# Kernel tuning notes

Hardware: AMD Instinct MI355X
Metric: run time of the kernel (lower is better)

The kernel has to match this reference:

```python
import jax, jax.numpy as jnp
from jax import lax
import numpy as np

B, T, F, H = 2048, 256, 64, 32


def setup_inputs() -> dict:
    key = jax.random.key(0)
    k = jax.random.split(key, 7)
    s_ih = 1.0 / np.sqrt(H)  # PyTorch GRU init scale uniform(-1/sqrt(H), 1/sqrt(H))
    return {
        "x": jax.random.normal(k[0], (B, T, F), dtype=jnp.float32),
        "W_ih": jax.random.uniform(k[1], (3 * H, F), minval=-s_ih, maxval=s_ih, dtype=jnp.float32),
        "W_hh": jax.random.uniform(k[2], (3 * H, H), minval=-s_ih, maxval=s_ih, dtype=jnp.float32),
        "b_ih": jax.random.uniform(k[3], (3 * H,), minval=-s_ih, maxval=s_ih, dtype=jnp.float32),
        "b_hh": jax.random.uniform(k[4], (3 * H,), minval=-s_ih, maxval=s_ih, dtype=jnp.float32),
        "W_head": jax.random.uniform(k[5], (1, H), minval=-s_ih, maxval=s_ih, dtype=jnp.float32),
        "b_head": jax.random.uniform(k[6], (1,), minval=-s_ih, maxval=s_ih, dtype=jnp.float32),
    }


def _gru_last_hidden(x, W_ih, W_hh, b_ih, b_hh):
    # Precompute input-to-gate projections for all timesteps: [B,T,3H] -> [T,B,3H]
    xg = jnp.einsum("btf,gf->btg", x, W_ih) + b_ih
    xg = jnp.moveaxis(xg, 1, 0)

    def step(h, xt):
        hg = h @ W_hh.T + b_hh  # [B,3H]
        xr, xz, xn = jnp.split(xt, 3, axis=-1)  # PyTorch gate order: r, z, n
        hr, hz, hn = jnp.split(hg, 3, axis=-1)
        r = jax.nn.sigmoid(xr + hr)
        z = jax.nn.sigmoid(xz + hz)
        n = jnp.tanh(xn + r * hn)
        h_new = (1.0 - z) * n + z * h
        return h_new, None

    h0 = jnp.zeros((x.shape[0], W_hh.shape[1]), dtype=x.dtype)
    hT, _ = lax.scan(step, h0, xg)
    return hT  # [B,H] == out[:, -1, :]


def reference(x, W_ih, W_hh, b_ih, b_hh, W_head, b_head):
    hT = _gru_last_hidden(x, W_ih, W_hh, b_ih, b_hh)
    y = hT @ W_head.T + b_head  # [B,1]
    return jax.nn.sigmoid(y)
```

## Files before the change

kernel.cpp:

```cpp
#include <hip/hip_runtime.h>
#include <cstdint>


#define TSEQ 256

typedef __attribute__((ext_vector_type(8))) short bf16x8;
typedef __attribute__((ext_vector_type(4))) float f32x4;
union BF8 { unsigned u[4]; bf16x8 v; };

__device__ __forceinline__ unsigned bfr(float f) {
    unsigned u = __float_as_uint(f);
    return u + 0x7fffu + ((u >> 16) & 1u);
}
__device__ __forceinline__ unsigned packhi(unsigned a, unsigned b) {
    return __builtin_amdgcn_perm(b, a, 0x07060302u);
}
__device__ __forceinline__ void cvt2(const float4& f0, const float4& f1,
                                     bf16x8& hi, bf16x8& lo) {
    float f[8] = {f0.x,f0.y,f0.z,f0.w, f1.x,f1.y,f1.z,f1.w};
    BF8 H, L;
    #pragma unroll
    for (int d = 0; d < 4; ++d) {
        float a = f[2*d], b = f[2*d+1];
        unsigned ua = __float_as_uint(a), ub = __float_as_uint(b);
        float ra = a - __uint_as_float(ua & 0xffff0000u);
        float rb = b - __uint_as_float(ub & 0xffff0000u);
        H.u[d] = packhi(ua, ub);
        L.u[d] = packhi(bfr(ra), bfr(rb));
    }
    hi = H.v; lo = L.v;
}
__device__ __forceinline__ float sel4(f32x4 v, int u) {
    float a = (u & 1) ? v[1] : v[0];
    float b = (u & 1) ? v[3] : v[2];
    return (u & 2) ? b : a;
}
__device__ __forceinline__ float sigx(float v) {
    return __builtin_amdgcn_rcpf(1.f + exp2f(-1.4426950408889634f * v));
}
__device__ __forceinline__ float tanhx(float v) {
    float e = exp2f(-2.8853900817779268f * fabsf(v));
    return copysignf((1.f - e) * __builtin_amdgcn_rcpf(1.f + e), v);
}

#define MFMA16(A, B, C) __builtin_amdgcn_mfma_f32_16x16x32_bf16((A), (B), (C), 0, 0, 0)

__global__ __launch_bounds__(128, 1)
void gru_fused(const float* __restrict__ x, const float* __restrict__ W_ih,
               const float* __restrict__ W_hh, const float* __restrict__ b_ih,
               const float* __restrict__ b_hh, const float* __restrict__ W_head,
               const float* __restrict__ b_head, float* __restrict__ out)
{
    __shared__ float xsh[2][1536];
    const int tid  = threadIdx.x;
    const int wid  = tid >> 6;
    const int lane = tid & 63;
    const int m = lane & 15, q = lane >> 4;
    const int bq = m & 3, u = m >> 2;
    const int b0 = blockIdx.x * 4;

    bf16x8 Aih[6][2];
    float4 ring[4];
    const float* xcol = x + ((size_t)(b0 + bq)*TSEQ + u)*64 + q*8;
    auto ldring = [&](int grp) {
        const float* p = xcol + grp*256;
        ring[0] = ((const float4*)p)[0];        ring[1] = ((const float4*)p)[1];
        ring[2] = ((const float4*)(p+32))[0];   ring[3] = ((const float4*)(p+32))[1];
    };
    auto projwrite = [&](int buf) {
        bf16x8 Xh0, Xl0, Xh1, Xl1;
        cvt2(ring[0], ring[1], Xh0, Xl0);
        cvt2(ring[2], ring[3], Xh1, Xl1);
        #pragma unroll
        for (int nt = 0; nt < 6; ++nt) {
            f32x4 a = MFMA16(Aih[nt][0], Xh0, ((f32x4){0.f,0.f,0.f,0.f}));
            a = MFMA16(Aih[nt][0], Xl0, a);
            a = MFMA16(Aih[nt][1], Xh1, a);
            a = MFMA16(Aih[nt][1], Xl1, a);
            *(f32x4*)&xsh[buf][lane*24 + nt*4] = a;
        }
    };

    bf16x8 Awh[6];
    f32x4 FRZ[4], BN0, BN1;
    float fn0 = 0.f, fn1 = 0.f;
    unsigned Hd[4] = {0u, 0u, 0u, 0u};
    float hOL = 0.f, hOH = 0.f;

    if (wid == 1) {
        #pragma unroll
        for (int nt = 0; nt < 6; ++nt)
            #pragma unroll
            for (int c = 0; c < 2; ++c) {
                const float* wp = W_ih + (nt*16 + m)*64 + c*32 + q*8;
                BF8 t;
                #pragma unroll
                for (int d = 0; d < 4; ++d) t.u[d] = packhi(bfr(wp[2*d]), bfr(wp[2*d+1]));
                Aih[nt][c] = t.v;
            }
        ldring(0);
        projwrite(0);
        ldring(1);
    } else {
        #pragma unroll
        for (int nt = 0; nt < 6; ++nt) {
            const float* wp = W_hh + (nt*16 + m)*32;
            BF8 t;
            #pragma unroll
            for (int d = 0; d < 4; ++d) {
                int dd = q*4 + d;
                t.u[d] = packhi(bfr(wp[dd]), bfr(wp[dd + 16]));
            }
            Awh[nt] = t.v;
        }
        #pragma unroll
        for (int nt = 0; nt < 4; ++nt) {
            f32x4 t;
            #pragma unroll
            for (int r = 0; r < 4; ++r) { int g = nt*16 + q*4 + r; t[r] = b_ih[g] + b_hh[g]; }
            FRZ[nt] = t;
        }
        #pragma unroll
        for (int r = 0; r < 4; ++r) { BN0[r] = b_hh[64+q*4+r]; BN1[r] = b_hh[80+q*4+r]; }
        fn0 = b_ih[64 + q*4 + u]; fn1 = b_ih[80 + q*4 + u];
    }
    __syncthreads();

    const int s0 = (q << 4) + bq;
    for (int g = 0; g < 64; ++g) {
        if (wid == 1) {
            if (g < 63) {
                projwrite((g + 1) & 1);
                ldring(g + 2 < 64 ? g + 2 : 63);
            }
        } else {
            const int cbuf = g & 1;
            float xp[4][6];
            #pragma unroll
            for (int s = 0; s < 4; ++s) {
                const float* rp = &xsh[cbuf][(s0 + 4*s)*24 + u];
                #pragma unroll
                for (int nt = 0; nt < 6; ++nt) xp[s][nt] = rp[nt*4];
            }
            #pragma unroll
            for (int s = 0; s < 4; ++s) {
                BF8 bh; bh.u[0]=Hd[0]; bh.u[1]=Hd[1]; bh.u[2]=Hd[2]; bh.u[3]=Hd[3];
                f32x4 a0 = MFMA16(Awh[0], bh.v, FRZ[0]);
                f32x4 a1 = MFMA16(Awh[1], bh.v, FRZ[1]);
                f32x4 a2 = MFMA16(Awh[2], bh.v, FRZ[2]);
                f32x4 a3 = MFMA16(Awh[3], bh.v, FRZ[3]);
                f32x4 a4 = MFMA16(Awh[4], bh.v, BN0);
                f32x4 a5 = MFMA16(Awh[5], bh.v, BN1);

                float r0 = sigx(xp[s][0] + sel4(a0, u));
                float r1 = sigx(xp[s][1] + sel4(a1, u));
                float z0 = sigx(xp[s][2] + sel4(a2, u));
                float z1 = sigx(xp[s][3] + sel4(a3, u));
                float t0 = tanhx(xp[s][4] + fn0 + r0 * sel4(a4, u));
                float t1 = tanhx(xp[s][5] + fn1 + r1 * sel4(a5, u));
                float hNL = t0 + z0 * (hOL - t0);
                float hNH = t1 + z1 * (hOH - t1);
                hOL = hNL; hOH = hNH;

                unsigned pk = packhi(bfr(hNL), bfr(hNH));
                #pragma unroll
                for (int w = 0; w < 4; ++w)
                    Hd[w] = (unsigned)__shfl((int)pk, s0 + (w << 2), 64);
            }
        }
        __syncthreads();
    }

    if (wid == 0) {
        float v = hOL * W_head[q*4 + u] + hOH * W_head[16 + q*4 + u];
        v += __shfl_xor(v, 4, 64);
        v += __shfl_xor(v, 8, 64);
        v += __shfl_xor(v, 16, 64);
        v += __shfl_xor(v, 32, 64);
        if (lane < 4) out[b0 + lane] = sigx(v + b_head[0]);
    }
}

extern "C" void kernel_launch(void* const* d_in, const int* in_sizes, int n_in,
                              void* d_out, int out_size, void* d_ws, size_t ws_size,
                              hipStream_t stream)
{
    const float* x      = (const float*)d_in[0];
    const float* W_ih   = (const float*)d_in[1];
    const float* W_hh   = (const float*)d_in[2];
    const float* b_ih   = (const float*)d_in[3];
    const float* b_hh   = (const float*)d_in[4];
    const float* W_head = (const float*)d_in[5];
    const float* b_head = (const float*)d_in[6];
    float* out = (float*)d_out;

    gru_fused<<<512, 128, 0, stream>>>(x, W_ih, W_hh, b_ih, b_hh,
                                       W_head, b_head, out);
}
```

Baseline: 255.0 us.

## Drop per-step cross-lane shuffles by computing all four gate rows per lane

The projected-input buffer in LDS now uses the MFMA C-fragment layout, so the recurrent wave can read whole f32x4 vectors instead of scalar gathers. Each lane now evaluates the gate activations for all four accumulator rows of its column. That lets it build the next bf16 hidden-state B operand directly and removes the sel4 selection and the four __shfl exchanges per timestep. Barriers are replaced with one that waits only on lgkmcnt. The cost is four times more sigmoid/tanh work per lane, computed redundantly across lanes.

```diff
diff --git a/kernel.cpp b/kernel.cpp
--- a/kernel.cpp
+++ b/kernel.cpp
@@ -30,11 +30,6 @@
     }
     hi = H.v; lo = L.v;
 }
-__device__ __forceinline__ float sel4(f32x4 v, int u) {
-    float a = (u & 1) ? v[1] : v[0];
-    float b = (u & 1) ? v[3] : v[2];
-    return (u & 2) ? b : a;
-}
 __device__ __forceinline__ float sigx(float v) {
     return __builtin_amdgcn_rcpf(1.f + exp2f(-1.4426950408889634f * v));
 }
@@ -44,6 +39,12 @@
 }
 
 #define MFMA16(A, B, C) __builtin_amdgcn_mfma_f32_16x16x32_bf16((A), (B), (C), 0, 0, 0)
+
+__device__ __forceinline__ void barrier_nodrain() {
+    asm volatile("s_waitcnt lgkmcnt(0)" ::: "memory");
+    __builtin_amdgcn_s_barrier();
+    asm volatile("" ::: "memory");
+}
 
 __global__ __launch_bounds__(128, 1)
 void gru_fused(const float* __restrict__ x, const float* __restrict__ W_ih,
@@ -77,15 +78,15 @@
             a = MFMA16(Aih[nt][0], Xl0, a);
             a = MFMA16(Aih[nt][1], Xh1, a);
             a = MFMA16(Aih[nt][1], Xl1, a);
-            *(f32x4*)&xsh[buf][lane*24 + nt*4] = a;
+            *(f32x4*)&xsh[buf][nt*256 + lane*4] = a;
         }
     };
 
     bf16x8 Awh[6];
-    f32x4 FRZ[4], BN0, BN1;
-    float fn0 = 0.f, fn1 = 0.f;
+    f32x4 FRZ[4], BN0, BN1, FN0, FN1;
     unsigned Hd[4] = {0u, 0u, 0u, 0u};
-    float hOL = 0.f, hOH = 0.f;
+    float hL[4] = {0.f,0.f,0.f,0.f};
+    float hH[4] = {0.f,0.f,0.f,0.f};
 
     if (wid == 1) {
         #pragma unroll
@@ -121,10 +122,12 @@
             FRZ[nt] = t;
         }
         #pragma unroll
-        for (int r = 0; r < 4; ++r) { BN0[r] = b_hh[64+q*4+r]; BN1[r] = b_hh[80+q*4+r]; }
-        fn0 = b_ih[64 + q*4 + u]; fn1 = b_ih[80 + q*4 + u];
-    }
-    __syncthreads();
+        for (int r = 0; r < 4; ++r) {
+            BN0[r] = b_hh[64+q*4+r]; BN1[r] = b_hh[80+q*4+r];
+            FN0[r] = b_ih[64+q*4+r]; FN1[r] = b_ih[80+q*4+r];
+        }
+    }
+    barrier_nodrain();
 
     const int s0 = (q << 4) + bq;
     for (int g = 0; g < 64; ++g) {
@@ -135,13 +138,13 @@
             }
         } else {
             const int cbuf = g & 1;
-            float xp[4][6];
-            #pragma unroll
-            for (int s = 0; s < 4; ++s) {
-                const float* rp = &xsh[cbuf][(s0 + 4*s)*24 + u];
+            f32x4 xpv[4][6];
+            #pragma unroll
+            for (int s = 0; s < 4; ++s)
                 #pragma unroll
-                for (int nt = 0; nt < 6; ++nt) xp[s][nt] = rp[nt*4];
-            }
+                for (int nt = 0; nt < 6; ++nt)
+                    xpv[s][nt] = *(const f32x4*)&xsh[cbuf][nt*256 + (s0 + 4*s)*4];
+
             #pragma unroll
             for (int s = 0; s < 4; ++s) {
                 BF8 bh; bh.u[0]=Hd[0]; bh.u[1]=Hd[1]; bh.u[2]=Hd[2]; bh.u[3]=Hd[3];
@@ -152,29 +155,29 @@
                 f32x4 a4 = MFMA16(Awh[4], bh.v, BN0);
                 f32x4 a5 = MFMA16(Awh[5], bh.v, BN1);
 
-                float r0 = sigx(xp[s][0] + sel4(a0, u));
-                float r1 = sigx(xp[s][1] + sel4(a1, u));
-                float z0 = sigx(xp[s][2] + sel4(a2, u));
-                float z1 = sigx(xp[s][3] + sel4(a3, u));
-                float t0 = tanhx(xp[s][4] + fn0 + r0 * sel4(a4, u));
-                float t1 = tanhx(xp[s][5] + fn1 + r1 * sel4(a5, u));
-                float hNL = t0 + z0 * (hOL - t0);
-                float hNH = t1 + z1 * (hOH - t1);
-                hOL = hNL; hOH = hNH;
-
-                unsigned pk = packhi(bfr(hNL), bfr(hNH));
                 #pragma unroll
-                for (int w = 0; w < 4; ++w)
-                    Hd[w] = (unsigned)__shfl((int)pk, s0 + (w << 2), 64);
-            }
-        }
-        __syncthreads();
+                for (int r = 0; r < 4; ++r) {
+                    float rL = sigx(xpv[s][0][r] + a0[r]);
+                    float rH = sigx(xpv[s][1][r] + a1[r]);
+                    float zL = sigx(xpv[s][2][r] + a2[r]);
+                    float zH = sigx(xpv[s][3][r] + a3[r]);
+                    float tL = tanhx(xpv[s][4][r] + FN0[r] + rL * a4[r]);
+                    float tH = tanhx(xpv[s][5][r] + FN1[r] + rH * a5[r]);
+                    float nL = tL + zL * (hL[r] - tL);
+                    float nH = tH + zH * (hH[r] - tH);
+                    hL[r] = nL; hH[r] = nH;
+                    Hd[r] = packhi(bfr(nL), bfr(nH));
+                }
+            }
+        }
+        barrier_nodrain();
     }
 
     if (wid == 0) {
-        float v = hOL * W_head[q*4 + u] + hOH * W_head[16 + q*4 + u];
-        v += __shfl_xor(v, 4, 64);
-        v += __shfl_xor(v, 8, 64);
+        float v = 0.f;
+        #pragma unroll
+        for (int r = 0; r < 4; ++r)
+            v += hL[r] * W_head[q*4 + r] + hH[r] * W_head[16 + q*4 + r];
         v += __shfl_xor(v, 16, 64);
         v += __shfl_xor(v, 32, 64);
         if (lane < 4) out[b0 + lane] = sigx(v + b_head[0]);
```

After: 364.1 us. 42.8% more time.

## Pack two batch quads per block, swap shuffles for DPP broadcast, lighter barriers

Applied to the files above, without the earlier changes.

Each block now handles 8 batch rows with 4 waves: two waves run the recurrence and two produce the input projections, launched as 256 blocks of 256 threads instead of 512 blocks of 128. The hidden-state exchange uses DPP quad broadcasts instead of ds_bpermute shuffles. The shared-memory layout is remapped with a padded stride, and barriers wait only on LDS counters so in-flight global loads are not drained. The aim is to shorten the serial per-step latency and the sync cost. In exchange, the grid has fewer blocks and the lane-to-row mapping changes, which could affect occupancy across CUs.

```diff
diff --git a/kernel.cpp b/kernel.cpp
--- a/kernel.cpp
+++ b/kernel.cpp
@@ -3,6 +3,7 @@
 
 
 #define TSEQ 256
+#define CSTRIDE 104
 
 typedef __attribute__((ext_vector_type(8))) short bf16x8;
 typedef __attribute__((ext_vector_type(4))) float f32x4;
@@ -45,49 +46,32 @@
 
 #define MFMA16(A, B, C) __builtin_amdgcn_mfma_f32_16x16x32_bf16((A), (B), (C), 0, 0, 0)
 
-__global__ __launch_bounds__(128, 1)
+#define QBCAST(x, w) ((unsigned)__builtin_amdgcn_update_dpp( \
+        0, (int)(x), ((w) | ((w)<<2) | ((w)<<4) | ((w)<<6)), 0xf, 0xf, true))
+
+__device__ __forceinline__ void barrier_nodrain() {
+    asm volatile("s_waitcnt lgkmcnt(0)" ::: "memory");
+    __builtin_amdgcn_s_barrier();
+    asm volatile("" ::: "memory");
+}
+
+__global__ __launch_bounds__(256, 1)
 void gru_fused(const float* __restrict__ x, const float* __restrict__ W_ih,
                const float* __restrict__ W_hh, const float* __restrict__ b_ih,
                const float* __restrict__ b_hh, const float* __restrict__ W_head,
                const float* __restrict__ b_head, float* __restrict__ out)
 {
-    __shared__ float xsh[2][1536];
+    __shared__ float xsh[2][2][16 * CSTRIDE];
     const int tid  = threadIdx.x;
     const int wid  = tid >> 6;
     const int lane = tid & 63;
     const int m = lane & 15, q = lane >> 4;
-    const int bq = m & 3, u = m >> 2;
-    const int b0 = blockIdx.x * 4;
-
-    bf16x8 Aih[6][2];
-    float4 ring[4];
-    const float* xcol = x + ((size_t)(b0 + bq)*TSEQ + u)*64 + q*8;
-    auto ldring = [&](int grp) {
-        const float* p = xcol + grp*256;
-        ring[0] = ((const float4*)p)[0];        ring[1] = ((const float4*)p)[1];
-        ring[2] = ((const float4*)(p+32))[0];   ring[3] = ((const float4*)(p+32))[1];
-    };
-    auto projwrite = [&](int buf) {
-        bf16x8 Xh0, Xl0, Xh1, Xl1;
-        cvt2(ring[0], ring[1], Xh0, Xl0);
-        cvt2(ring[2], ring[3], Xh1, Xl1);
-        #pragma unroll
-        for (int nt = 0; nt < 6; ++nt) {
-            f32x4 a = MFMA16(Aih[nt][0], Xh0, ((f32x4){0.f,0.f,0.f,0.f}));
-            a = MFMA16(Aih[nt][0], Xl0, a);
-            a = MFMA16(Aih[nt][1], Xh1, a);
-            a = MFMA16(Aih[nt][1], Xl1, a);
-            *(f32x4*)&xsh[buf][lane*24 + nt*4] = a;
-        }
-    };
-
-    bf16x8 Awh[6];
-    f32x4 FRZ[4], BN0, BN1;
-    float fn0 = 0.f, fn1 = 0.f;
-    unsigned Hd[4] = {0u, 0u, 0u, 0u};
-    float hOL = 0.f, hOH = 0.f;
-
-    if (wid == 1) {
+    const int b0 = blockIdx.x * 8;
+
+    if (wid >= 2) {
+        const int pq = wid - 2;
+        const int bq = m & 3, u = m >> 2;
+        bf16x8 Aih[6][2];
         #pragma unroll
         for (int nt = 0; nt < 6; ++nt)
             #pragma unroll
@@ -98,10 +82,41 @@
                 for (int d = 0; d < 4; ++d) t.u[d] = packhi(bfr(wp[2*d]), bfr(wp[2*d+1]));
                 Aih[nt][c] = t.v;
             }
+        float4 ring[4];
+        const float* xcol = x + ((size_t)(b0 + pq*4 + bq)*TSEQ + u)*64 + q*8;
+        auto ldring = [&](int grp) {
+            const float* p = xcol + grp*256;
+            ring[0] = ((const float4*)p)[0];        ring[1] = ((const float4*)p)[1];
+            ring[2] = ((const float4*)(p+32))[0];   ring[3] = ((const float4*)(p+32))[1];
+        };
+        auto projwrite = [&](int buf) {
+            bf16x8 Xh0, Xl0, Xh1, Xl1;
+            cvt2(ring[0], ring[1], Xh0, Xl0);
+            cvt2(ring[2], ring[3], Xh1, Xl1);
+            #pragma unroll
+            for (int nt = 0; nt < 6; ++nt) {
+                f32x4 a = MFMA16(Aih[nt][0], Xh0, ((f32x4){0.f,0.f,0.f,0.f}));
+                a = MFMA16(Aih[nt][0], Xl0, a);
+                a = MFMA16(Aih[nt][1], Xh1, a);
+                a = MFMA16(Aih[nt][1], Xl1, a);
+                *(f32x4*)&xsh[buf][pq][m*CSTRIDE + nt*16 + q*4] = a;
+            }
+        };
         ldring(0);
         projwrite(0);
         ldring(1);
+        barrier_nodrain();
+        for (int g = 0; g < 64; ++g) {
+            if (g < 63) {
+                projwrite((g + 1) & 1);
+                ldring(g + 2 < 64 ? g + 2 : 63);
+            }
+            barrier_nodrain();
+        }
     } else {
+        const int cq = wid;
+        const int bq = m >> 2, u = m & 3;
+        bf16x8 Awh[6];
         #pragma unroll
         for (int nt = 0; nt < 6; ++nt) {
             const float* wp = W_hh + (nt*16 + m)*32;
@@ -113,6 +128,7 @@
             }
             Awh[nt] = t.v;
         }
+        f32x4 FRZ[4], BN0, BN1;
         #pragma unroll
         for (int nt = 0; nt < 4; ++nt) {
             f32x4 t;
@@ -122,25 +138,20 @@
         }
         #pragma unroll
         for (int r = 0; r < 4; ++r) { BN0[r] = b_hh[64+q*4+r]; BN1[r] = b_hh[80+q*4+r]; }
-        fn0 = b_ih[64 + q*4 + u]; fn1 = b_ih[80 + q*4 + u];
-    }
-    __syncthreads();
-
-    const int s0 = (q << 4) + bq;
-    for (int g = 0; g < 64; ++g) {
-        if (wid == 1) {
-            if (g < 63) {
-                projwrite((g + 1) & 1);
-                ldring(g + 2 < 64 ? g + 2 : 63);
-            }
-        } else {
+        const float fn0 = b_ih[64 + q*4 + u], fn1 = b_ih[80 + q*4 + u];
+
+        unsigned Hd[4] = {0u, 0u, 0u, 0u};
+        float hOL = 0.f, hOH = 0.f;
+        barrier_nodrain();
+
+        for (int g = 0; g < 64; ++g) {
             const int cbuf = g & 1;
             float xp[4][6];
             #pragma unroll
             for (int s = 0; s < 4; ++s) {
-                const float* rp = &xsh[cbuf][(s0 + 4*s)*24 + u];
+                const float* rp = &xsh[cbuf][cq][(bq + 4*s)*CSTRIDE + q*4 + u];
                 #pragma unroll
-                for (int nt = 0; nt < 6; ++nt) xp[s][nt] = rp[nt*4];
+                for (int nt = 0; nt < 6; ++nt) xp[s][nt] = rp[nt*16];
             }
             #pragma unroll
             for (int s = 0; s < 4; ++s) {
@@ -163,21 +174,21 @@
                 hOL = hNL; hOH = hNH;
 
                 unsigned pk = packhi(bfr(hNL), bfr(hNH));
-                #pragma unroll
-                for (int w = 0; w < 4; ++w)
-                    Hd[w] = (unsigned)__shfl((int)pk, s0 + (w << 2), 64);
-            }
-        }
-        __syncthreads();
-    }
-
-    if (wid == 0) {
+                Hd[0] = QBCAST(pk, 0);
+                Hd[1] = QBCAST(pk, 1);
+                Hd[2] = QBCAST(pk, 2);
+                Hd[3] = QBCAST(pk, 3);
+            }
+            barrier_nodrain();
+        }
+
         float v = hOL * W_head[q*4 + u] + hOH * W_head[16 + q*4 + u];
-        v += __shfl_xor(v, 4, 64);
-        v += __shfl_xor(v, 8, 64);
+        v += __shfl_xor(v, 1, 64);
+        v += __shfl_xor(v, 2, 64);
         v += __shfl_xor(v, 16, 64);
         v += __shfl_xor(v, 32, 64);
-        if (lane < 4) out[b0 + lane] = sigx(v + b_head[0]);
+        if (lane < 16 && (lane & 3) == 0)
+            out[b0 + cq*4 + (lane >> 2)] = sigx(v + b_head[0]);
     }
 }
 
@@ -194,6 +205,6 @@
     const float* b_head = (const float*)d_in[6];
     float* out = (float*)d_out;
 
-    gru_fused<<<512, 128, 0, stream>>>(x, W_ih, W_hh, b_ih, b_hh,
+    gru_fused<<<256, 256, 0, stream>>>(x, W_ih, W_hh, b_ih, b_hh,
                                        W_head, b_head, out);
 }
```

After: 239.4 us. -6.1%, faster.
